# Kernel optimization log

Hardware: AMD Instinct MI355X
Metric: run time of the kernel (lower is better)

## Reference

```python
import jax, jax.numpy as jnp
import numpy as np

INF = 1e9  # large finite sentinel (avoid inf arithmetic in potentials)


def _hungarian(cost):
    """Exact linear sum assignment (Jonker-Volgenant style shortest augmenting
    path, O(N^3)) on a single [N, N] cost matrix. Returns col_ind (int32 [N])
    such that row i is matched to column col_ind[i] with minimal total cost
    (same solution as scipy.optimize.linear_sum_assignment up to ties).
    Column index n is a virtual 'start' column (e-maxx formulation)."""
    n = cost.shape[0]

    def row_body(i, carry):
        u, v, p = carry  # u: row potentials [n]; v: col potentials [n+1]; p[j]: row assigned to col j (-1 free)
        p = p.at[n].set(i)
        state = (u, v, p,
                 jnp.full(n + 1, INF, cost.dtype),   # minv
                 jnp.zeros(n + 1, dtype=bool),       # used
                 jnp.zeros(n + 1, dtype=jnp.int32),  # way (parent col on path)
                 jnp.int32(n))                       # j0 current col

        def cond(st):
            _, _, p_, _, _, _, j0 = st
            return p_[j0] >= 0  # stop when we reach a free column

        def body(st):
            u_, v_, p_, minv, used, way, j0 = st
            used = used.at[j0].set(True)
            i0 = p_[j0]
            cur = cost[i0] - u_[i0] - v_[:n]          # reduced costs of row i0 [n]
            cur = jnp.where(used[:n], INF, cur)
            better = cur < minv[:n]
            minv = minv.at[:n].set(jnp.where(better, cur, minv[:n]))
            way = way.at[:n].set(jnp.where(better, j0, way[:n]))
            masked = jnp.where(used[:n], INF, minv[:n])
            j1 = jnp.argmin(masked).astype(jnp.int32)
            delta = masked[j1]
            # dual update: used cols raise row potential, others shrink minv
            u_ = u_.at[p_].add(jnp.where(used, delta, jnp.zeros((), cost.dtype)))
            v_ = jnp.where(used, v_ - delta, v_)
            minv = jnp.where(used, minv, minv - delta)
            return (u_, v_, p_, minv, used, way, j1)

        u, v, p, _, _, way, j0 = jax.lax.while_loop(cond, body, state)

        # augment along the alternating path back to the virtual column
        def cond2(s):
            j, _ = s
            return j != n

        def body2(s):
            j, p_ = s
            j_prev = way[j]
            return j_prev, p_.at[j].set(p_[j_prev])

        _, p = jax.lax.while_loop(cond2, body2, (j0, p))
        return (u, v, p)

    u0 = jnp.zeros(n, cost.dtype)
    v0 = jnp.zeros(n + 1, cost.dtype)
    p0 = jnp.full(n + 1, -1, dtype=jnp.int32)
    _, _, p = jax.lax.fori_loop(0, n, row_body, (u0, v0, p0))
    # p[j] = row matched to col j  ->  col_ind[row] = j
    col_ind = jnp.zeros(n, jnp.int32).at[p[:n]].set(jnp.arange(n, dtype=jnp.int32))
    return col_ind


def setup_inputs() -> dict:
    key = jax.random.key(0)
    k1, k2 = jax.random.split(key)
    B, N, D = 2048, 24, 256
    slots = jax.random.normal(k1, (B, N, D), dtype=jnp.float32)
    prev_slots = jax.random.normal(k2, (B, N, D), dtype=jnp.float32)
    return {"slots": slots, "prev_slots": prev_slots}


def reference(slots, prev_slots):
    """HungarianPredictor.forward with similarity='cosine': reorder current
    slots to align with prev_slots ordering via optimal 1-1 matching."""
    eps = 1e-12  # torch F.normalize eps
    pn = prev_slots / jnp.maximum(
        jnp.linalg.norm(prev_slots, axis=-1, keepdims=True), eps)
    cn = slots / jnp.maximum(
        jnp.linalg.norm(slots, axis=-1, keepdims=True), eps)
    # cost[b, i, j] = 1 - <prev_i, curr_j>   [B, N, N]
    cost = 1.0 - jnp.einsum('bnd,bmd->bnm', pn, cn)
    col = jax.vmap(_hungarian)(jax.lax.stop_gradient(cost))  # [B, N] int32
    reordered = jax.vmap(lambda s, c: s[c])(slots, col)       # gather per batch
    return reordered
```

## Files before the change

kernel.cpp:

```cpp
#include <hip/hip_runtime.h>
#include <math.h>

#define N    24
#define D    256
#define BLK  256
#define NB   4
#define CTS  28
#define INFV 1e9f

__device__ __forceinline__ int rl_i(int x, int l) {
    return __builtin_amdgcn_readlane(x, l);
}
__device__ __forceinline__ float rl_f(float x, int l) {
    return __uint_as_float((unsigned)__builtin_amdgcn_readlane((int)__float_as_uint(x), l));
}
__device__ __forceinline__ float fmin2(float a, float b) { return a < b ? a : b; }

__device__ __forceinline__ float dpp_min32(float x) {
    int t;
    t = __builtin_amdgcn_update_dpp(__float_as_int(x), __float_as_int(x), 0xB1,  0xF, 0xF, false);
    x = fmin2(__int_as_float(t), x);
    t = __builtin_amdgcn_update_dpp(__float_as_int(x), __float_as_int(x), 0x4E,  0xF, 0xF, false);
    x = fmin2(__int_as_float(t), x);
    t = __builtin_amdgcn_update_dpp(__float_as_int(x), __float_as_int(x), 0x114, 0xF, 0xF, false);
    x = fmin2(__int_as_float(t), x);
    t = __builtin_amdgcn_update_dpp(__float_as_int(x), __float_as_int(x), 0x118, 0xF, 0xF, false);
    x = fmin2(__int_as_float(t), x);
    t = __builtin_amdgcn_update_dpp(__float_as_int(x), __float_as_int(x), 0x142, 0xF, 0xF, false);
    x = fmin2(__int_as_float(t), x);
    return x;
}

__device__ __forceinline__ float sel24(const float (&cq)[24], int s) {
    switch (s) {
        case 0:  return cq[0];  case 1:  return cq[1];
        case 2:  return cq[2];  case 3:  return cq[3];
        case 4:  return cq[4];  case 5:  return cq[5];
        case 6:  return cq[6];  case 7:  return cq[7];
        case 8:  return cq[8];  case 9:  return cq[9];
        case 10: return cq[10]; case 11: return cq[11];
        case 12: return cq[12]; case 13: return cq[13];
        case 14: return cq[14]; case 15: return cq[15];
        case 16: return cq[16]; case 17: return cq[17];
        case 18: return cq[18]; case 19: return cq[19];
        case 20: return cq[20]; case 21: return cq[21];
        case 22: return cq[22]; default: return cq[23];
    }
}

#define DOT4(a, b) ((a).x*(b).x + (a).y*(b).y + (a).z*(b).z + (a).w*(b).w)
#define LGKM0() __asm__ volatile("s_waitcnt lgkmcnt(0)" ::: "memory")

__global__ __launch_bounds__(BLK, 2) void hungarian_fused(
    const float* __restrict__ slots,
    const float* __restrict__ prev,
    float* __restrict__ out, int B)
{
    __shared__ __align__(16) float costT[NB][N][CTS];
    __shared__ int winner[NB][N];
    __shared__ int colw[NB][N];

    const int tid  = threadIdx.x;
    const int lane = tid & 63;
    const int wv   = tid >> 6;
    const int bw   = blockIdx.x * NB + wv;
    if (bw >= B) return;

    const int rg = lane >> 3;
    const int cg = lane & 7;
    const float4* pA = (const float4*)(prev  + (size_t)bw * N * D) + rg * 3 * (D / 4);
    const float4* pC = (const float4*)(slots + (size_t)bw * N * D) + cg * 3 * (D / 4);

    float s00=0,s01=0,s02=0,s10=0,s11=0,s12=0,s20=0,s21=0,s22=0;
    float pa0=0,pa1=0,pa2=0,pc0=0,pc1=0,pc2=0;
    #pragma unroll 4
    for (int k = 0; k < 64; ++k) {
        float4 a0 = pA[k], a1 = pA[64+k], a2 = pA[128+k];
        float4 b0 = pC[k], b1 = pC[64+k], b2 = pC[128+k];
        s00 += DOT4(a0,b0); s01 += DOT4(a0,b1); s02 += DOT4(a0,b2);
        s10 += DOT4(a1,b0); s11 += DOT4(a1,b1); s12 += DOT4(a1,b2);
        s20 += DOT4(a2,b0); s21 += DOT4(a2,b1); s22 += DOT4(a2,b2);
        pa0 += DOT4(a0,a0); pa1 += DOT4(a1,a1); pa2 += DOT4(a2,a2);
        pc0 += DOT4(b0,b0); pc1 += DOT4(b1,b1); pc2 += DOT4(b2,b2);
    }
    float ira0 = 1.0f / fmaxf(sqrtf(pa0), 1e-12f);
    float ira1 = 1.0f / fmaxf(sqrtf(pa1), 1e-12f);
    float ira2 = 1.0f / fmaxf(sqrtf(pa2), 1e-12f);
    float irc0 = 1.0f / fmaxf(sqrtf(pc0), 1e-12f);
    float irc1 = 1.0f / fmaxf(sqrtf(pc1), 1e-12f);
    float irc2 = 1.0f / fmaxf(sqrtf(pc2), 1e-12f);

    {
        float* ct = &costT[wv][0][0];
        const int cb = cg * 3, rb = rg * 3;
        ct[(cb+0)*CTS + rb+0] = 1.0f - s00*ira0*irc0;
        ct[(cb+1)*CTS + rb+0] = 1.0f - s01*ira0*irc1;
        ct[(cb+2)*CTS + rb+0] = 1.0f - s02*ira0*irc2;
        ct[(cb+0)*CTS + rb+1] = 1.0f - s10*ira1*irc0;
        ct[(cb+1)*CTS + rb+1] = 1.0f - s11*ira1*irc1;
        ct[(cb+2)*CTS + rb+1] = 1.0f - s12*ira1*irc2;
        ct[(cb+0)*CTS + rb+2] = 1.0f - s20*ira2*irc0;
        ct[(cb+1)*CTS + rb+2] = 1.0f - s21*ira2*irc1;
        ct[(cb+2)*CTS + rb+2] = 1.0f - s22*ira2*irc2;
    }
    LGKM0();

    const bool isCol = (lane < N);
    const int  jj    = isCol ? lane : 0;
    float cq[24];
    {
        const float4* cp4 = (const float4*)&costT[wv][jj][0];
        #pragma unroll
        for (int r = 0; r < 6; ++r) {
            float4 q = cp4[r];
            cq[r*4+0] = q.x; cq[r*4+1] = q.y; cq[r*4+2] = q.z; cq[r*4+3] = q.w;
        }
    }

    float cm = cq[0]; int ri = 0;
    #pragma unroll
    for (int i = 1; i < N; ++i) { if (cq[i] < cm) { cm = cq[i]; ri = i; } }

    if (isCol) winner[wv][lane] = -1;
    LGKM0();
    if (isCol) winner[wv][ri] = lane;
    LGKM0();
    int p = -1;
    if (isCol && winner[wv][ri] == lane) p = ri;
    const int widx = isCol ? lane : 0;
    unsigned long long mm = __ballot(isCol && winner[wv][widx] >= 0);
    unsigned freeRows = (~(unsigned)mm) & ((1u << N) - 1);

    float uu = 0.0f;
    float v  = isCol ? cm : INFV;
    int  way = -1;

    {
        int steps = 0;
        while (freeRows && steps < 40) {
            ++steps;
            int f = (int)__builtin_ctz(freeRows);
            float cif = sel24(cq, f);
            float rc  = isCol ? (cif - v) : INFV;
            float u1  = rl_f(dpp_min32(rc), 31);
            unsigned long long e1 = __ballot(rc == u1);
            int j1 = (int)__builtin_ctzll(e1);
            float rc2 = (lane == j1) ? INFV : rc;
            float u2  = rl_f(dpp_min32(rc2), 31);
            if (lane == f) uu = u2;
            if (lane == j1 && u1 < u2) v -= (u2 - u1);
            int iold = rl_i(p, j1);
            if (lane == j1) p = f;
            freeRows &= ~(1u << f);
            if (iold >= 0) freeRows |= (1u << iold);
        }
    }

    int guard = 0;
    while (freeRows && guard < 1500) {
        const int f = (int)__builtin_ctz(freeRows);
        freeRows &= freeRows - 1;

        float minv  = INFV;
        bool  used  = false;
        bool  inTree = false;
        int   s_j0 = -1;
        int   s_i0 = f;
        int   j1   = 0;

        while (guard++ < 1500) {
            inTree = inTree || (lane == s_i0);
            used   = used   || (lane == s_j0);

            float cij = sel24(cq, s_i0);
            float u0  = rl_f(uu, s_i0);
            float cur = cij - u0 - v;
            bool  act = isCol && !used;
            if (act && cur < minv) { minv = cur; way = s_j0; }
            float masked = act ? minv : INFV;

            float delta = rl_f(dpp_min32(masked), 31);
            unsigned long long eq = __ballot(masked == delta);
            int j1s = (int)__builtin_ctzll(eq);

            if (inTree) uu += delta;
            if (used) v -= delta;
            else if (act) minv -= delta;

            int i0n = rl_i(p, j1s);
            if (i0n < 0) { j1 = j1s; break; }
            s_j0 = j1s; s_i0 = i0n;
        }

        int jcur = j1, asteps = 0;
        while (asteps++ < 32) {
            int wj   = rl_i(way, jcur);
            int pnew = (wj < 0) ? f : rl_i(p, wj);
            if (lane == jcur) p = pnew;
            if (wj < 0) break;
            jcur = wj;
        }
    }

    if (isCol) colw[wv][p] = lane;
    LGKM0();

    const float4* sg4 = (const float4*)(slots + (size_t)bw * N * D);
    float4*       og4 = (float4*)(out + (size_t)bw * N * D);
    #pragma unroll
    for (int i = 0; i < N; ++i) {
        int c = colw[wv][i];
        og4[i * 64 + lane] = sg4[c * 64 + lane];
    }
}

extern "C" void kernel_launch(void* const* d_in, const int* in_sizes, int n_in,
                              void* d_out, int out_size, void* d_ws, size_t ws_size,
                              hipStream_t stream) {
    const float* slots = (const float*)d_in[0];
    const float* prev  = (const float*)d_in[1];
    float* out = (float*)d_out;
    int B = in_sizes[0] / (N * D);
    int grid = (B + NB - 1) / NB;
    hungarian_fused<<<grid, BLK, 0, stream>>>(slots, prev, out, B);
}
```

Before: 209.5 us.

## Use one wave per block, read cost from LDS, drop auction warm start

Each batch element now runs in its own 64-thread block instead of four waves per 256-thread block, and the launch-bounds minimum-occupancy hint is removed. The per-lane 24-entry register copy of the cost column and its switch-based selection are replaced by direct LDS reads of a row-major cost matrix padded to 25 columns. The greedy pre-assignment (auction-style warm start) loop is removed, so the shortest-path phase may need more augmentations. Loop guards become fixed-count loops, which cuts register pressure and branch code but adds an LDS load to every Dijkstra step.

```diff
diff --git a/kernel.cpp b/kernel.cpp
--- a/kernel.cpp
+++ b/kernel.cpp
@@ -1,11 +1,8 @@
 #include <hip/hip_runtime.h>
-#include <math.h>
 
 #define N    24
 #define D    256
-#define BLK  256
-#define NB   4
-#define CTS  28
+#define CS   25
 #define INFV 1e9f
 
 __device__ __forceinline__ int rl_i(int x, int l) {
@@ -31,39 +28,20 @@
     return x;
 }
 
-__device__ __forceinline__ float sel24(const float (&cq)[24], int s) {
-    switch (s) {
-        case 0:  return cq[0];  case 1:  return cq[1];
-        case 2:  return cq[2];  case 3:  return cq[3];
-        case 4:  return cq[4];  case 5:  return cq[5];
-        case 6:  return cq[6];  case 7:  return cq[7];
-        case 8:  return cq[8];  case 9:  return cq[9];
-        case 10: return cq[10]; case 11: return cq[11];
-        case 12: return cq[12]; case 13: return cq[13];
-        case 14: return cq[14]; case 15: return cq[15];
-        case 16: return cq[16]; case 17: return cq[17];
-        case 18: return cq[18]; case 19: return cq[19];
-        case 20: return cq[20]; case 21: return cq[21];
-        case 22: return cq[22]; default: return cq[23];
-    }
-}
-
 #define DOT4(a, b) ((a).x*(b).x + (a).y*(b).y + (a).z*(b).z + (a).w*(b).w)
 #define LGKM0() __asm__ volatile("s_waitcnt lgkmcnt(0)" ::: "memory")
 
-__global__ __launch_bounds__(BLK, 2) void hungarian_fused(
+__global__ __launch_bounds__(64) void hungarian_fused(
     const float* __restrict__ slots,
     const float* __restrict__ prev,
     float* __restrict__ out, int B)
 {
-    __shared__ __align__(16) float costT[NB][N][CTS];
-    __shared__ int winner[NB][N];
-    __shared__ int colw[NB][N];
+    __shared__ __align__(16) float cost[N * CS];
+    __shared__ int winner[N];
+    __shared__ int colw[N];
 
-    const int tid  = threadIdx.x;
-    const int lane = tid & 63;
-    const int wv   = tid >> 6;
-    const int bw   = blockIdx.x * NB + wv;
+    const int lane = threadIdx.x;
+    const int bw   = blockIdx.x;
     if (bw >= B) return;
 
     const int rg = lane >> 3;
@@ -91,88 +69,54 @@
     float irc2 = 1.0f / fmaxf(sqrtf(pc2), 1e-12f);
 
     {
-        float* ct = &costT[wv][0][0];
-        const int cb = cg * 3, rb = rg * 3;
-        ct[(cb+0)*CTS + rb+0] = 1.0f - s00*ira0*irc0;
-        ct[(cb+1)*CTS + rb+0] = 1.0f - s01*ira0*irc1;
-        ct[(cb+2)*CTS + rb+0] = 1.0f - s02*ira0*irc2;
-        ct[(cb+0)*CTS + rb+1] = 1.0f - s10*ira1*irc0;
-        ct[(cb+1)*CTS + rb+1] = 1.0f - s11*ira1*irc1;
-        ct[(cb+2)*CTS + rb+1] = 1.0f - s12*ira1*irc2;
-        ct[(cb+0)*CTS + rb+2] = 1.0f - s20*ira2*irc0;
-        ct[(cb+1)*CTS + rb+2] = 1.0f - s21*ira2*irc1;
-        ct[(cb+2)*CTS + rb+2] = 1.0f - s22*ira2*irc2;
+        const int rb = rg * 3, cb = cg * 3;
+        cost[(rb+0)*CS + cb+0] = 1.0f - s00*ira0*irc0;
+        cost[(rb+0)*CS + cb+1] = 1.0f - s01*ira0*irc1;
+        cost[(rb+0)*CS + cb+2] = 1.0f - s02*ira0*irc2;
+        cost[(rb+1)*CS + cb+0] = 1.0f - s10*ira1*irc0;
+        cost[(rb+1)*CS + cb+1] = 1.0f - s11*ira1*irc1;
+        cost[(rb+1)*CS + cb+2] = 1.0f - s12*ira1*irc2;
+        cost[(rb+2)*CS + cb+0] = 1.0f - s20*ira2*irc0;
+        cost[(rb+2)*CS + cb+1] = 1.0f - s21*ira2*irc1;
+        cost[(rb+2)*CS + cb+2] = 1.0f - s22*ira2*irc2;
     }
     LGKM0();
 
     const bool isCol = (lane < N);
-    const int  jj    = isCol ? lane : 0;
-    float cq[24];
-    {
-        const float4* cp4 = (const float4*)&costT[wv][jj][0];
-        #pragma unroll
-        for (int r = 0; r < 6; ++r) {
-            float4 q = cp4[r];
-            cq[r*4+0] = q.x; cq[r*4+1] = q.y; cq[r*4+2] = q.z; cq[r*4+3] = q.w;
-        }
+    const int  jc    = isCol ? lane : 23;
+
+    float cm = INFV; int ri = 0;
+    #pragma unroll
+    for (int i = 0; i < N; ++i) {
+        float c = cost[i * CS + jc];
+        if (c < cm) { cm = c; ri = i; }
     }
-
-    float cm = cq[0]; int ri = 0;
-    #pragma unroll
-    for (int i = 1; i < N; ++i) { if (cq[i] < cm) { cm = cq[i]; ri = i; } }
-
-    if (isCol) winner[wv][lane] = -1;
+    if (isCol) winner[lane] = -1;
     LGKM0();
-    if (isCol) winner[wv][ri] = lane;
+    if (isCol) winner[ri] = lane;
     LGKM0();
     int p = -1;
-    if (isCol && winner[wv][ri] == lane) p = ri;
-    const int widx = isCol ? lane : 0;
-    unsigned long long mm = __ballot(isCol && winner[wv][widx] >= 0);
+    if (isCol && winner[ri] == lane) p = ri;
+    unsigned long long mm = __ballot(isCol && winner[lane] >= 0);
     unsigned freeRows = (~(unsigned)mm) & ((1u << N) - 1);
 
     float uu = 0.0f;
     float v  = isCol ? cm : INFV;
     int  way = -1;
 
-    {
-        int steps = 0;
-        while (freeRows && steps < 40) {
-            ++steps;
-            int f = (int)__builtin_ctz(freeRows);
-            float cif = sel24(cq, f);
-            float rc  = isCol ? (cif - v) : INFV;
-            float u1  = rl_f(dpp_min32(rc), 31);
-            unsigned long long e1 = __ballot(rc == u1);
-            int j1 = (int)__builtin_ctzll(e1);
-            float rc2 = (lane == j1) ? INFV : rc;
-            float u2  = rl_f(dpp_min32(rc2), 31);
-            if (lane == f) uu = u2;
-            if (lane == j1 && u1 < u2) v -= (u2 - u1);
-            int iold = rl_i(p, j1);
-            if (lane == j1) p = f;
-            freeRows &= ~(1u << f);
-            if (iold >= 0) freeRows |= (1u << iold);
-        }
-    }
-
-    int guard = 0;
-    while (freeRows && guard < 1500) {
+    while (freeRows) {
         const int f = (int)__builtin_ctz(freeRows);
         freeRows &= freeRows - 1;
 
-        float minv  = INFV;
-        bool  used  = false;
-        bool  inTree = false;
-        int   s_j0 = -1;
-        int   s_i0 = f;
-        int   j1   = 0;
+        float minv = INFV;
+        bool  used = false, inTree = false;
+        int   s_j0 = -1, s_i0 = f, j1 = 0;
 
-        while (guard++ < 1500) {
-            inTree = inTree || (lane == s_i0);
-            used   = used   || (lane == s_j0);
-
-            float cij = sel24(cq, s_i0);
+        #pragma unroll 1
+        for (int it = 0; it < 26; ++it) {
+            float cij = cost[s_i0 * CS + jc];
+            inTree |= (lane == s_i0);
+            used   |= (lane == s_j0);
             float u0  = rl_f(uu, s_i0);
             float cur = cij - u0 - v;
             bool  act = isCol && !used;
@@ -181,19 +125,20 @@
 
             float delta = rl_f(dpp_min32(masked), 31);
             unsigned long long eq = __ballot(masked == delta);
-            int j1s = (int)__builtin_ctzll(eq);
+            j1 = (int)__builtin_ctzll(eq);
 
             if (inTree) uu += delta;
             if (used) v -= delta;
             else if (act) minv -= delta;
 
-            int i0n = rl_i(p, j1s);
-            if (i0n < 0) { j1 = j1s; break; }
-            s_j0 = j1s; s_i0 = i0n;
+            int i0n = rl_i(p, j1);
+            if (i0n < 0) break;
+            s_j0 = j1; s_i0 = i0n;
         }
 
-        int jcur = j1, asteps = 0;
-        while (asteps++ < 32) {
+        int jcur = j1;
+        #pragma unroll 1
+        for (int as = 0; as < 26; ++as) {
             int wj   = rl_i(way, jcur);
             int pnew = (wj < 0) ? f : rl_i(p, wj);
             if (lane == jcur) p = pnew;
@@ -202,14 +147,14 @@
         }
     }
 
-    if (isCol) colw[wv][p] = lane;
+    if (isCol) colw[p] = lane;
     LGKM0();
 
     const float4* sg4 = (const float4*)(slots + (size_t)bw * N * D);
     float4*       og4 = (float4*)(out + (size_t)bw * N * D);
     #pragma unroll
     for (int i = 0; i < N; ++i) {
-        int c = colw[wv][i];
+        int c = colw[i];
         og4[i * 64 + lane] = sg4[c * 64 + lane];
     }
 }
@@ -221,6 +166,5 @@
     const float* prev  = (const float*)d_in[1];
     float* out = (float*)d_out;
     int B = in_sizes[0] / (N * D);
-    int grid = (B + NB - 1) / NB;
-    hungarian_fused<<<grid, BLK, 0, stream>>>(slots, prev, out, B);
+    hungarian_fused<<<B, 64, 0, stream>>>(slots, prev, out, B);
 }
```

After: 198.4 us. -5.3%, faster.
